# Optimization experiments

Measured on AMD Instinct MI355X. Metric: run time of the kernel, lower is better.

## Reference

```python
import jax, jax.numpy as jnp
import numpy as np
from jax import lax

B = 256
L = 1024
C = 64           # num_inputs == num_channels[l]
NUM_LAYERS = 5
KERNEL = 3
HID = 256
NUM_STATIC = 32
OUT_DIM = 2
KQ = 24576
T_TEMP = 0.07
NUM_NEIGHBORS = 1
EPS = 1e-12


def _l2n(x, axis):
    n = jnp.linalg.norm(x, axis=axis, keepdims=True)
    return x / jnp.maximum(n, EPS)


def _causal_conv(x, w, b, dil):
    # x: [B, C, L], w: [O, I, K] -> left-pad (K-1)*dil == Conv1d(pad both)+Chomp1d
    y = lax.conv_general_dilated(x, w, window_strides=(1,),
                                 padding=[((KERNEL - 1) * dil, 0)],
                                 rhs_dilation=(dil,),
                                 dimension_numbers=('NCH', 'OIH', 'NCH'))
    return y + b[None, :, None]


def _tcn(x, c1w, c1b, c2w, c2b):
    # stacked TemporalBlocks, dilation 2**l, identity residual (in==out channels)
    for l in range(NUM_LAYERS):
        d = 2 ** l
        h = jax.nn.relu(_causal_conv(x, c1w[l], c1b[l], d))
        h = jax.nn.relu(_causal_conv(h, c2w[l], c2b[l], d))
        x = jax.nn.relu(h + x)
    return x


def _mlp(x, w1, b1, w2, b2):
    # Linear -> ReLU -> Linear (use_batch_norm=False, eval: no dropout)
    return jax.nn.relu(x @ w1 + b1) @ w2 + b2


def setup_inputs() -> dict:
    key = jax.random.key(0)
    ks = jax.random.split(key, 24)
    d = {}
    d['sequence_q_s'] = jax.random.normal(ks[0], (B, L, C), jnp.float32)
    d['sequence_k_s'] = jax.random.normal(ks[1], (B, L, C), jnp.float32)
    d['static_s'] = jax.random.normal(ks[2], (B, NUM_STATIC), jnp.float32)
    d['sequence_q_t'] = jax.random.normal(ks[3], (B, L, C), jnp.float32)
    d['sequence_k_t'] = jax.random.normal(ks[4], (B, L, C), jnp.float32)
    d['static_t'] = jax.random.normal(ks[5], (B, NUM_STATIC), jnp.float32)
    d['alpha'] = jnp.ones((1,), jnp.float32)
    cs = 1.0 / np.sqrt(C * KERNEL)
    d['c1w'] = jax.random.normal(ks[6], (NUM_LAYERS, C, C, KERNEL), jnp.float32) * cs
    d['c1b'] = jnp.zeros((NUM_LAYERS, C), jnp.float32)
    d['c2w'] = jax.random.normal(ks[7], (NUM_LAYERS, C, C, KERNEL), jnp.float32) * cs
    d['c2b'] = jnp.zeros((NUM_LAYERS, C), jnp.float32)
    d['pjw1'] = jax.random.normal(ks[8], (C, HID), jnp.float32) / np.sqrt(C)
    d['pjb1'] = jnp.zeros((HID,), jnp.float32)
    d['pjw2'] = jax.random.normal(ks[9], (HID, C), jnp.float32) / np.sqrt(HID)
    d['pjb2'] = jnp.zeros((C,), jnp.float32)
    d['prw1'] = jax.random.normal(ks[10], (C + NUM_STATIC, HID), jnp.float32) / np.sqrt(C + NUM_STATIC)
    d['prb1'] = jnp.zeros((HID,), jnp.float32)
    d['prw2'] = jax.random.normal(ks[11], (HID, OUT_DIM), jnp.float32) / np.sqrt(HID)
    d['prb2'] = jnp.zeros((OUT_DIM,), jnp.float32)
    d['dw1'] = jax.random.normal(ks[12], (C, HID), jnp.float32) / np.sqrt(C)
    d['db1'] = jnp.zeros((HID,), jnp.float32)
    d['dw2'] = jax.random.normal(ks[13], (HID, 1), jnp.float32) / np.sqrt(HID)
    d['db2'] = jnp.zeros((1,), jnp.float32)
    qs = jax.random.normal(ks[14], (C, KQ), jnp.float32)
    qt = jax.random.normal(ks[15], (C, KQ), jnp.float32)
    d['queue_s'] = _l2n(qs, 0)
    d['queue_t'] = _l2n(qt, 0)
    return d


def reference(sequence_q_s, sequence_k_s, static_s, sequence_q_t, sequence_k_t, static_t, alpha,
              c1w, c1b, c2w, c2b, pjw1, pjb1, pjw2, pjb2, prw1, prb1, prw2, prb2,
              dw1, db1, dw2, db2, queue_s, queue_t):
    sg = lax.stop_gradient

    def encode(seq):  # [B, L, C] -> normalized [B, C]
        return _l2n(_tcn(jnp.transpose(seq, (0, 2, 1)), c1w, c1b, c2w, c2b)[:, :, -1], 1)

    q_s = encode(sequence_q_s)
    p_q_s = _l2n(_mlp(q_s, pjw1, pjb1, pjw2, pjb2), 1)
    q_t = encode(sequence_q_t)
    p_q_t = _l2n(_mlp(q_t, pjw1, pjb1, pjw2, pjb2), 1)
    # key encoder under no_grad (params equal to query encoder at init)
    k_s = sg(encode(sequence_k_s))
    k_t = sg(encode(sequence_k_t))

    logits_s = jnp.concatenate([p_q_s @ k_s.T, p_q_s @ sg(queue_s)], axis=1) / T_TEMP
    labels_s = jnp.arange(B, dtype=jnp.int32)
    logits_t = jnp.concatenate([p_q_t @ k_t.T, p_q_t @ sg(queue_t)], axis=1) / T_TEMP
    labels_t = jnp.arange(B, dtype=jnp.int32)

    # NN(k_t, q_s.detach()): cdist + topk smallest -> pseudo labels
    q_s_det = sg(q_s)
    d2 = (jnp.sum(k_t * k_t, 1)[:, None] + jnp.sum(q_s_det * q_s_det, 1)[None, :]
          - 2.0 * (k_t @ q_s_det.T))  # [B_t, B_s]
    _, idx = lax.top_k(-d2, NUM_NEIGHBORS)
    labels_ts = idx[:, 0]

    logits_ts = (q_t @ q_s_det.T) / T_TEMP

    labels_domain = jnp.concatenate([jnp.ones((B, 1), jnp.float32), jnp.zeros((B, 1), jnp.float32)], 0)
    # gradient reversal is identity in forward
    q_rev = jnp.concatenate([q_s, q_t], axis=0)
    pred_domain = _mlp(q_rev, dw1, db1, dw2, db2)

    y_s = _mlp(jnp.concatenate([q_s, static_s], axis=1), prw1, prb1, prw2, prb2)

    return (logits_s, labels_s, logits_t, labels_t, logits_ts, labels_ts,
            pred_domain, labels_domain, y_s)
```

## Files before the change

kernel.cpp:

```cpp
#include <hip/hip_runtime.h>
#include <hip/hip_bf16.h>

#define B_SZ   256
#define L_SZ   1024
#define C_SZ   64
#define HID    256
#define KQ     24576
#define WIN    125
#define WSTART (L_SZ - WIN)

#define OFF_LOGITS_S   0LL
#define OFF_LABELS_S   6356992LL
#define OFF_LOGITS_T   6357248LL
#define OFF_LABELS_T   12714240LL
#define OFF_LOGITS_TS  12714496LL
#define OFF_LABELS_TS  12780032LL
#define OFF_PRED_DOM   12780288LL
#define OFF_LABELS_DOM 12780800LL
#define OFF_YS         12781312LL

#define INV_T (1.0f / 0.07f)

typedef __attribute__((ext_vector_type(8))) short  bf16x8;
typedef __attribute__((ext_vector_type(4))) float  floatx4;
typedef __attribute__((ext_vector_type(16))) float floatx16;
typedef __attribute__((ext_vector_type(4))) unsigned short ushortx4;

__device__ __forceinline__ unsigned short f2bf_rne(float x) {
    unsigned u = __float_as_uint(x);
    unsigned r = u + 0x7fffu + ((u >> 16) & 1u);
    return (unsigned short)(r >> 16);
}
__device__ __forceinline__ float bf2f(unsigned short h) {
    return __uint_as_float(((unsigned)h) << 16);
}

__device__ __forceinline__ int swz2(int r) { return ((r >> 1) & 7) << 4; }

__global__ void prep_frag_kernel(const float* __restrict__ c1w,
                                 const float* __restrict__ c2w,
                                 unsigned short* __restrict__ wf) {
    int bid = blockIdx.x;
    int kb = bid & 1, mt = (bid >> 1) & 3;
    int sttap = bid >> 3;
    int tap = sttap % 3, st = sttap / 3;
    int l = st >> 1, cv = st & 1;
    int tid = threadIdx.x;
    int j = tid & 7, lane = tid >> 3;
    int co = mt * 16 + (lane & 15);
    int ci = kb * 32 + (lane >> 4) * 8 + j;
    const float* src = cv ? c2w : c1w;
    float w = src[((l * 64 + co) * 64 + ci) * 3 + tap];
    unsigned short hi = f2bf_rne(w);
    unsigned short lo = f2bf_rne(w - bf2f(hi));
    size_t b0 = ((((size_t)((st * 3 + tap) * 2 + 0)) * 4 + mt) * 2 + kb) * 512 + lane * 8 + j;
    size_t b1 = ((((size_t)((st * 3 + tap) * 2 + 1)) * 4 + mt) * 2 + kb) * 512 + lane * 8 + j;
    wf[b0] = hi;
    wf[b1] = lo;
}

#define R0H 0
#define R0L 16384
#define R1H 32768
#define R1L 40960
#define HHB 49152
#define HLB 65536
#define SCRATCH_B 57344

template<bool RES, bool FINAL>
__device__ __forceinline__ void conv_pass(
    char* lds, const bf16x8* __restrict__ wf8,
    int st, int inH, int inL, int rows_valid, int stride,
    int outH, int outL, int n_out, int tiles,
    int resH, int resL, int res_valid,
    const float* __restrict__ bias,
    int mt, int lg, int li, int lane)
{
    bf16x8 A[3][2][2];
#pragma unroll
    for (int tap = 0; tap < 3; ++tap)
#pragma unroll
        for (int h = 0; h < 2; ++h)
#pragma unroll
            for (int kb = 0; kb < 2; ++kb)
                A[tap][h][kb] = wf8[((((st * 3 + tap) * 2 + h) * 4 + mt) * 2 + kb) * 64 + lane];

    int co0 = mt * 16 + lg * 4;
    float4 b4 = *(const float4*)(bias + co0);
    float ba[4] = {b4.x, b4.y, b4.z, b4.w};

    for (int tt = 0; tt < tiles; ++tt) {
        int i = tt * 16 + li;
        floatx4 acc = {0.f, 0.f, 0.f, 0.f};
#pragma unroll
        for (int tap = 0; tap < 3; ++tap) {
            int jr = i * stride + tap;
            jr = (jr < rows_valid - 1) ? jr : (rows_valid - 1);
            int sw = swz2(jr);
            const char* pH = lds + inH + jr * 128;
            const char* pL = lds + inL + jr * 128;
#pragma unroll
            for (int kb = 0; kb < 2; ++kb) {
                int cb = (kb * 64 + lg * 16) ^ sw;
                bf16x8 bH = *(const bf16x8*)(pH + cb);
                bf16x8 bL = *(const bf16x8*)(pL + cb);
                acc = __builtin_amdgcn_mfma_f32_16x16x32_bf16(A[tap][0][kb], bH, acc, 0, 0, 0);
                acc = __builtin_amdgcn_mfma_f32_16x16x32_bf16(A[tap][0][kb], bL, acc, 0, 0, 0);
                acc = __builtin_amdgcn_mfma_f32_16x16x32_bf16(A[tap][1][kb], bH, acc, 0, 0, 0);
            }
        }
        float v[4];
#pragma unroll
        for (int r = 0; r < 4; ++r) v[r] = fmaxf(acc[r] + ba[r], 0.f);
        if (RES) {
            int rr = 2 * i + 4;
            rr = (rr < res_valid - 1) ? rr : (res_valid - 1);
            int rsw = swz2(rr);
            int rcb = (mt * 32 + lg * 8) ^ rsw;
            ushortx4 rh = *(const ushortx4*)(lds + resH + rr * 128 + rcb);
            ushortx4 rl = *(const ushortx4*)(lds + resL + rr * 128 + rcb);
#pragma unroll
            for (int r = 0; r < 4; ++r)
                v[r] = fmaxf(v[r] + bf2f(rh[r]) + bf2f(rl[r]), 0.f);
        }
        if (FINAL) {
            if (i == 0) {
                float* scratch = (float*)(lds + SCRATCH_B);
#pragma unroll
                for (int r = 0; r < 4; ++r) scratch[co0 + r] = v[r];
            }
        } else {
            if (i < n_out) {
                ushortx4 h4, l4;
#pragma unroll
                for (int r = 0; r < 4; ++r) {
                    unsigned short hh = f2bf_rne(v[r]);
                    h4[r] = (short)hh;
                    l4[r] = (short)f2bf_rne(v[r] - bf2f(hh));
                }
                int wsw = swz2(i);
                int wcb = (mt * 32 + lg * 8) ^ wsw;
                *(ushortx4*)(lds + outH + i * 128 + wcb) = h4;
                *(ushortx4*)(lds + outL + i * 128 + wcb) = l4;
            }
        }
    }
}

__launch_bounds__(256)
__global__ void encode_kernel(const float* __restrict__ sqs, const float* __restrict__ sks,
                              const float* __restrict__ sqt, const float* __restrict__ skt,
                              const unsigned short* __restrict__ wf,
                              const float* __restrict__ c1b, const float* __restrict__ c2b,
                              const float* __restrict__ pjw1, const float* __restrict__ pjb1,
                              const float* __restrict__ pjw2, const float* __restrict__ pjb2,
                              float* __restrict__ enc, float* __restrict__ proj,
                              unsigned short* __restrict__ pbf) {
    __shared__ char lds[81920];
    int b = blockIdx.x;
    int s = blockIdx.y;
    const float* seq = (s == 0) ? sqs : (s == 1) ? sks : (s == 2) ? sqt : skt;
    const float4* base4 = reinterpret_cast<const float4*>(seq + ((size_t)b * L_SZ + WSTART) * C_SZ);
    int tid = threadIdx.x;

    for (int idx = tid; idx < 2000; idx += 256) {
        float4 v = base4[idx];
        int t = idx >> 4, c0 = (idx & 15) * 4;
        int cb = (c0 * 2) ^ swz2(t);
        float vv[4] = {v.x, v.y, v.z, v.w};
        ushortx4 h4, l4;
#pragma unroll
        for (int r = 0; r < 4; ++r) {
            unsigned short hh = f2bf_rne(vv[r]);
            h4[r] = (short)hh;
            l4[r] = (short)f2bf_rne(vv[r] - bf2f(hh));
        }
        *(ushortx4*)(lds + R0H + t * 128 + cb) = h4;
        *(ushortx4*)(lds + R0L + t * 128 + cb) = l4;
    }
    __syncthreads();

    int mt   = tid >> 6;
    int lane = tid & 63;
    int lg = lane >> 4, li = lane & 15;
    const bf16x8* wf8 = (const bf16x8*)wf;

    const int n_in[5] = {125, 61, 29, 13, 5};
    const int n1a[5]  = {123, 59, 27, 11, 3};
    const int n2a[5]  = {61, 29, 13, 5, 1};
    const int t1a[5]  = {8, 4, 2, 1, 1};
    const int t2a[5]  = {4, 2, 1, 1, 1};

#pragma unroll
    for (int l = 0; l < 5; ++l) {
        int xH = (l & 1) ? R1H : R0H, xL = (l & 1) ? R1L : R0L;
        int yH = (l & 1) ? R0H : R1H, yL = (l & 1) ? R0L : R1L;
        conv_pass<false, false>(lds, wf8, l * 2, xH, xL, n_in[l], 1,
                                HHB, HLB, n1a[l], t1a[l], 0, 0, 0,
                                c1b + l * 64, mt, lg, li, lane);
        __syncthreads();
        if (l < 4) {
            conv_pass<true, false>(lds, wf8, l * 2 + 1, HHB, HLB, n1a[l], 2,
                                   yH, yL, n2a[l], t2a[l], xH, xL, n_in[l],
                                   c2b + l * 64, mt, lg, li, lane);
        } else {
            conv_pass<true, true>(lds, wf8, l * 2 + 1, HHB, HLB, n1a[l], 2,
                                  yH, yL, n2a[l], t2a[l], xH, xL, n_in[l],
                                  c2b + l * 64, mt, lg, li, lane);
        }
        __syncthreads();
    }

    float* xn = (float*)(lds + R0H);
    if (tid < 64) {
        float vv = ((float*)(lds + SCRATCH_B))[tid];
        float sq = vv * vv;
#pragma unroll
        for (int off = 32; off; off >>= 1) sq += __shfl_xor(sq, off, 64);
        float norm = fmaxf(sqrtf(sq), 1e-12f);
        float nv = vv / norm;
        enc[((size_t)s * B_SZ + b) * 64 + tid] = nv;
        xn[tid] = nv;
    }
    __syncthreads();

    if (s == 0 || s == 2) {
        float* hv   = (float*)(lds + R1H);
        float* red4 = (float*)(lds + R1H + 1024);
        {
            float acc = pjb1[tid];
            const float* wcol = pjw1 + tid;
            for (int c = 0; c < 64; ++c) acc = fmaf(xn[c], wcol[c * 256], acc);
            hv[tid] = fmaxf(acc, 0.f);
        }
        __syncthreads();
        {
            int wv = tid >> 6, o = tid & 63;
            float acc = 0.f;
            const float* wcol = pjw2 + o;
            int j0 = wv * 64;
            for (int j = j0; j < j0 + 64; ++j) acc = fmaf(hv[j], wcol[j * 64], acc);
            red4[wv * 64 + o] = acc;
        }
        __syncthreads();
        if (tid < 64) {
            float o = pjb2[tid];
#pragma unroll
            for (int k = 0; k < 4; ++k) o += red4[k * 64 + tid];
            float sq = o * o;
#pragma unroll
            for (int off = 32; off; off >>= 1) sq += __shfl_xor(sq, off, 64);
            float norm = fmaxf(sqrtf(sq), 1e-12f);
            float pv = o / norm;
            int which = s >> 1;
            proj[((size_t)which * B_SZ + b) * 64 + tid] = pv;
            pbf[((size_t)which * B_SZ + b) * 64 + tid] = f2bf_rne(pv);
        }
    }
}

__launch_bounds__(512)
__global__ void qlogits_kernel(const float* __restrict__ proj,
                               const unsigned short* __restrict__ pbf,
                               const float* __restrict__ enc,
                               const float* __restrict__ queue_s, const float* __restrict__ queue_t,
                               float* __restrict__ out) {
    __shared__ char lds[8448];
    int bx = blockIdx.x;
    int sz = blockIdx.y;
    int tid = threadIdx.x;
    long long outBase0 = (sz == 0) ? OFF_LOGITS_S : OFF_LOGITS_T;

    if (bx >= 384) {
        float (*pt)[65] = (float(*)[65])lds;
        int rt = bx - 384;
        const float* p = proj + ((size_t)sz * B_SZ + rt * 32) * 64;
        for (int idx = tid; idx < 32 * 64; idx += 512) {
            pt[idx >> 6][idx & 63] = p[idx];
        }
        __syncthreads();
        if (tid < 256) {
            float acc[32];
#pragma unroll
            for (int r = 0; r < 32; ++r) acc[r] = 0.f;
            int j = tid;
            const float* k = enc + ((size_t)(sz == 0 ? 1 : 3) * B_SZ + j) * 64;
            for (int c = 0; c < 64; ++c) {
                float bv = k[c];
#pragma unroll
                for (int r = 0; r < 32; ++r) acc[r] = fmaf(pt[r][c], bv, acc[r]);
            }
#pragma unroll
            for (int r = 0; r < 32; ++r) {
                out[outBase0 + (long long)(rt * 32 + r) * 24832 + j] = acc[r] * INV_T;
            }
        }
        return;
    }

    int j0 = bx * 64;
    const float* q = (sz == 0 ? queue_s : queue_t);

    {
#pragma unroll
        for (int pass = 0; pass < 2; ++pass) {
            int idx = pass * 512 + tid;
            int c = idx >> 4, jj0 = (idx & 15) * 4;
            float4 v = *(const float4*)(q + (size_t)c * KQ + j0 + jj0);
            float vv[4] = {v.x, v.y, v.z, v.w};
#pragma unroll
            for (int r = 0; r < 4; ++r) {
                int jj = jj0 + r;
                *(unsigned short*)(lds + jj * 128 + ((c * 2) ^ ((jj & 7) << 4))) = f2bf_rne(vv[r]);
            }
        }
    }
    __syncthreads();

    int w = tid >> 6, lane = tid & 63;
    int r31 = lane & 31, hi = lane >> 5;
    int arow = w * 32 + r31;
    const bf16x8* pa = (const bf16x8*)(pbf + ((size_t)sz * B_SZ + arow) * 64);
    bf16x8 A[4];
#pragma unroll
    for (int ks = 0; ks < 4; ++ks)
        A[ks] = pa[ks * 2 + hi];
    long long outBase = outBase0 + 256 + j0;
#pragma unroll
    for (int ct = 0; ct < 2; ++ct) {
        int col = ct * 32 + r31;
        bf16x8 Bf[4];
#pragma unroll
        for (int ks = 0; ks < 4; ++ks)
            Bf[ks] = *(const bf16x8*)(lds + col * 128 + (((ks * 16 + hi * 8) * 2) ^ ((col & 7) << 4)));
        floatx16 acc;
#pragma unroll
        for (int r = 0; r < 16; ++r) acc[r] = 0.f;
#pragma unroll
        for (int ks = 0; ks < 4; ++ks)
            acc = __builtin_amdgcn_mfma_f32_32x32x16_bf16(A[ks], Bf[ks], acc, 0, 0, 0);
#pragma unroll
        for (int r = 0; r < 16; ++r) {
            int drow = (r & 3) + 8 * (r >> 2) + 4 * hi;
            out[outBase + (long long)(w * 32 + drow) * 24832 + ct * 32 + r31] = acc[r] * INV_T;
        }
    }
}

__global__ void heads_kernel(const float* __restrict__ enc, const float* __restrict__ stat,
                             const float* __restrict__ dw1, const float* __restrict__ db1,
                             const float* __restrict__ dw2, const float* __restrict__ db2,
                             const float* __restrict__ prw1, const float* __restrict__ prb1,
                             const float* __restrict__ prw2, const float* __restrict__ prb2,
                             float* __restrict__ out) {
    int bx = blockIdx.x;
    int tid = threadIdx.x;

    if (bx < 256) {
        __shared__ float kt[64];
        __shared__ float qt[64];
        __shared__ float swv[4];
        __shared__ int   swj[4];
        int i = bx;
        if (tid < 64) {
            kt[tid] = enc[((size_t)3 * B_SZ + i) * 64 + tid];
            qt[tid] = enc[((size_t)2 * B_SZ + i) * 64 + tid];
        }
        __syncthreads();
        int j = tid;
        const float* qs = enc + (size_t)j * 64;
        float dkt = 0.f, dqt = 0.f, qq = 0.f, kk = 0.f;
        for (int c = 0; c < 64; ++c) {
            float v = qs[c];
            dkt = fmaf(kt[c], v, dkt);
            dqt = fmaf(qt[c], v, dqt);
            qq  = fmaf(v, v, qq);
            kk  = fmaf(kt[c], kt[c], kk);
        }
        out[OFF_LOGITS_TS + (long long)i * 256 + j] = dqt * INV_T;
        float d2 = kk + qq - 2.f * dkt;
        float bv = d2; int bj = j;
#pragma unroll
        for (int off = 32; off; off >>= 1) {
            float ov = __shfl_xor(bv, off, 64);
            int   oj = __shfl_xor(bj, off, 64);
            if (ov < bv || (ov == bv && oj < bj)) { bv = ov; bj = oj; }
        }
        int w = tid >> 6;
        if ((tid & 63) == 0) { swv[w] = bv; swj[w] = bj; }
        __syncthreads();
        if (tid == 0) {
            float best = swv[0]; int bi = swj[0];
#pragma unroll
            for (int k = 1; k < 4; ++k)
                if (swv[k] < best || (swv[k] == best && swj[k] < bi)) { best = swv[k]; bi = swj[k]; }
            out[OFF_LABELS_TS + i] = (float)bi;
        }
    } else if (bx < 768) {
        __shared__ float xv[64];
        __shared__ float red[256];
        int r = bx - 256;
        const float* x = enc + ((r < 256) ? ((size_t)0 * B_SZ + r) : ((size_t)2 * B_SZ + (r - 256))) * 64;
        if (tid < 64) xv[tid] = x[tid];
        __syncthreads();
        float h = db1[tid];
        for (int c = 0; c < 64; ++c) h = fmaf(xv[c], dw1[c * 256 + tid], h);
        h = fmaxf(h, 0.f);
        red[tid] = h * dw2[tid];
        __syncthreads();
        for (int s = 128; s; s >>= 1) {
            if (tid < s) red[tid] += red[tid + s];
            __syncthreads();
        }
        if (tid == 0) out[OFF_PRED_DOM + r] = red[0] + db2[0];
    } else if (bx < 1024) {
        __shared__ float xv[96];
        __shared__ float red[256];
        int b = bx - 768;
        if (tid < 64)       xv[tid] = enc[(size_t)b * 64 + tid];
        else if (tid < 96)  xv[tid] = stat[(size_t)b * 32 + (tid - 64)];
        __syncthreads();
        float h = prb1[tid];
        for (int c = 0; c < 96; ++c) h = fmaf(xv[c], prw1[c * 256 + tid], h);
        h = fmaxf(h, 0.f);
        for (int o = 0; o < 2; ++o) {
            red[tid] = h * prw2[tid * 2 + o];
            __syncthreads();
            for (int s = 128; s; s >>= 1) {
                if (tid < s) red[tid] += red[tid + s];
                __syncthreads();
            }
            if (tid == 0) out[OFF_YS + (long long)b * 2 + o] = red[0] + prb2[o];
            __syncthreads();
        }
    } else {
        int t = (bx - 1024) * 256 + tid;
        if (t < 256) {
            out[OFF_LABELS_S + t] = (float)t;
            out[OFF_LABELS_T + t] = (float)t;
        }
        if (t < 512) out[OFF_LABELS_DOM + t] = (t < 256) ? 1.f : 0.f;
    }
}

extern "C" void kernel_launch(void* const* d_in, const int* in_sizes, int n_in,
                              void* d_out, int out_size, void* d_ws, size_t ws_size,
                              hipStream_t stream) {
    const float* sqs    = (const float*)d_in[0];
    const float* sks    = (const float*)d_in[1];
    const float* stat_s = (const float*)d_in[2];
    const float* sqt    = (const float*)d_in[3];
    const float* skt    = (const float*)d_in[4];
    const float* c1w    = (const float*)d_in[7];
    const float* c1b    = (const float*)d_in[8];
    const float* c2w    = (const float*)d_in[9];
    const float* c2b    = (const float*)d_in[10];
    const float* pjw1   = (const float*)d_in[11];
    const float* pjb1   = (const float*)d_in[12];
    const float* pjw2   = (const float*)d_in[13];
    const float* pjb2   = (const float*)d_in[14];
    const float* prw1   = (const float*)d_in[15];
    const float* prb1   = (const float*)d_in[16];
    const float* prw2   = (const float*)d_in[17];
    const float* prb2   = (const float*)d_in[18];
    const float* dw1    = (const float*)d_in[19];
    const float* db1    = (const float*)d_in[20];
    const float* dw2    = (const float*)d_in[21];
    const float* db2    = (const float*)d_in[22];
    const float* queue_s = (const float*)d_in[23];
    const float* queue_t = (const float*)d_in[24];

    float* out = (float*)d_out;
    unsigned short* wf = (unsigned short*)d_ws;
    float* enc  = (float*)((char*)d_ws + 491520);
    float* proj = enc + 65536;
    unsigned short* pbf = (unsigned short*)(proj + 32768);

    prep_frag_kernel<<<240, 512, 0, stream>>>(c1w, c2w, wf);
    encode_kernel<<<dim3(256, 4), 256, 0, stream>>>(sqs, sks, sqt, skt, wf, c1b, c2b,
                                                    pjw1, pjb1, pjw2, pjb2, enc, proj, pbf);
    qlogits_kernel<<<dim3(392, 2), 512, 0, stream>>>(proj, pbf, enc, queue_s, queue_t, out);
    heads_kernel<<<1026, 256, 0, stream>>>(enc, stat_s, dw1, db1, dw2, db2,
                                           prw1, prb1, prw2, prb2, out);
}
```

Baseline: 89.23 us.

## Split TCN encoder into two kernels, batching four sequences per block for late layers

The encoder kernel is split in two. The first kernel runs layers 0-1 per sequence and spills the layer-2 input (29 rows, split into hi and lo bf16 halves) into the output buffer as scratch. The second kernel packs four sequences per block for layers 2-4 and the projection MLP, so the tiny late layers with only one or two tiles no longer leave most waves idle. The price is an extra launch and a global round trip, and the LDS swizzle is changed from pairs of rows to single rows.

```diff
diff --git a/kernel.cpp b/kernel.cpp
--- a/kernel.cpp
+++ b/kernel.cpp
@@ -35,7 +35,7 @@
     return __uint_as_float(((unsigned)h) << 16);
 }
 
-__device__ __forceinline__ int swz2(int r) { return ((r >> 1) & 7) << 4; }
+__device__ __forceinline__ int swzl(int r) { return (r & 7) << 4; }
 
 __global__ void prep_frag_kernel(const float* __restrict__ c1w,
                                  const float* __restrict__ c2w,
@@ -65,97 +65,104 @@
 #define R1L 40960
 #define HHB 49152
 #define HLB 65536
-#define SCRATCH_B 57344
 
 template<bool RES, bool FINAL>
-__device__ __forceinline__ void conv_pass(
-    char* lds, const bf16x8* __restrict__ wf8,
-    int st, int inH, int inL, int rows_valid, int stride,
+__device__ __forceinline__ void conv_tile(
+    char* L, const bf16x8 A[3][2][2],
+    int inH, int inL, int rows_valid, int stride,
+    int outH, int outL, int n_out, int scrOff,
+    int resH, int resL, int res_valid,
+    const float ba[4], int i, int mt, int lg)
+{
+    floatx4 acc = {0.f, 0.f, 0.f, 0.f};
+#pragma unroll
+    for (int tap = 0; tap < 3; ++tap) {
+        int jr = i * stride + tap;
+        jr = (jr < rows_valid - 1) ? jr : (rows_valid - 1);
+        int sw = swzl(jr);
+        const char* pH = L + inH + jr * 128;
+        const char* pL = L + inL + jr * 128;
+#pragma unroll
+        for (int kb = 0; kb < 2; ++kb) {
+            int cb = (kb * 64 + lg * 16) ^ sw;
+            bf16x8 bH = *(const bf16x8*)(pH + cb);
+            bf16x8 bL = *(const bf16x8*)(pL + cb);
+            acc = __builtin_amdgcn_mfma_f32_16x16x32_bf16(A[tap][0][kb], bH, acc, 0, 0, 0);
+            acc = __builtin_amdgcn_mfma_f32_16x16x32_bf16(A[tap][0][kb], bL, acc, 0, 0, 0);
+            acc = __builtin_amdgcn_mfma_f32_16x16x32_bf16(A[tap][1][kb], bH, acc, 0, 0, 0);
+        }
+    }
+    float v[4];
+#pragma unroll
+    for (int r = 0; r < 4; ++r) v[r] = fmaxf(acc[r] + ba[r], 0.f);
+    if (RES) {
+        int rr = 2 * i + 4;
+        rr = (rr < res_valid - 1) ? rr : (res_valid - 1);
+        int rcb = (mt * 32 + lg * 8) ^ swzl(rr);
+        ushortx4 rh = *(const ushortx4*)(L + resH + rr * 128 + rcb);
+        ushortx4 rl = *(const ushortx4*)(L + resL + rr * 128 + rcb);
+#pragma unroll
+        for (int r = 0; r < 4; ++r)
+            v[r] = fmaxf(v[r] + bf2f(rh[r]) + bf2f(rl[r]), 0.f);
+    }
+    if (FINAL) {
+        if (i == 0) {
+            float* scr = (float*)(L + scrOff);
+            int co0 = mt * 16 + lg * 4;
+#pragma unroll
+            for (int r = 0; r < 4; ++r) scr[co0 + r] = v[r];
+        }
+    } else if (i < n_out) {
+        ushortx4 h4, l4;
+#pragma unroll
+        for (int r = 0; r < 4; ++r) {
+            unsigned short hh = f2bf_rne(v[r]);
+            h4[r] = (short)hh;
+            l4[r] = (short)f2bf_rne(v[r] - bf2f(hh));
+        }
+        int wcb = (mt * 32 + lg * 8) ^ swzl(i);
+        *(ushortx4*)(L + outH + i * 128 + wcb) = h4;
+        *(ushortx4*)(L + outL + i * 128 + wcb) = l4;
+    }
+}
+
+__device__ __forceinline__ void loadAfrag(bf16x8 A[3][2][2], const bf16x8* __restrict__ wf8,
+                                          int st, int mt, int lane) {
+#pragma unroll
+    for (int tap = 0; tap < 3; ++tap)
+#pragma unroll
+        for (int h = 0; h < 2; ++h)
+#pragma unroll
+            for (int kb = 0; kb < 2; ++kb)
+                A[tap][h][kb] = wf8[((((st * 3 + tap) * 2 + h) * 4 + mt) * 2 + kb) * 64 + lane];
+}
+
+template<bool RES>
+__device__ __forceinline__ void conv_passA(
+    char* lds, const bf16x8* __restrict__ wf8, int st,
+    int inH, int inL, int rows_valid, int stride,
     int outH, int outL, int n_out, int tiles,
     int resH, int resL, int res_valid,
-    const float* __restrict__ bias,
-    int mt, int lg, int li, int lane)
+    const float* __restrict__ bias, int mt, int lg, int li, int lane)
 {
     bf16x8 A[3][2][2];
-#pragma unroll
-    for (int tap = 0; tap < 3; ++tap)
-#pragma unroll
-        for (int h = 0; h < 2; ++h)
-#pragma unroll
-            for (int kb = 0; kb < 2; ++kb)
-                A[tap][h][kb] = wf8[((((st * 3 + tap) * 2 + h) * 4 + mt) * 2 + kb) * 64 + lane];
-
+    loadAfrag(A, wf8, st, mt, lane);
     int co0 = mt * 16 + lg * 4;
     float4 b4 = *(const float4*)(bias + co0);
     float ba[4] = {b4.x, b4.y, b4.z, b4.w};
-
     for (int tt = 0; tt < tiles; ++tt) {
-        int i = tt * 16 + li;
-        floatx4 acc = {0.f, 0.f, 0.f, 0.f};
-#pragma unroll
-        for (int tap = 0; tap < 3; ++tap) {
-            int jr = i * stride + tap;
-            jr = (jr < rows_valid - 1) ? jr : (rows_valid - 1);
-            int sw = swz2(jr);
-            const char* pH = lds + inH + jr * 128;
-            const char* pL = lds + inL + jr * 128;
-#pragma unroll
-            for (int kb = 0; kb < 2; ++kb) {
-                int cb = (kb * 64 + lg * 16) ^ sw;
-                bf16x8 bH = *(const bf16x8*)(pH + cb);
-                bf16x8 bL = *(const bf16x8*)(pL + cb);
-                acc = __builtin_amdgcn_mfma_f32_16x16x32_bf16(A[tap][0][kb], bH, acc, 0, 0, 0);
-                acc = __builtin_amdgcn_mfma_f32_16x16x32_bf16(A[tap][0][kb], bL, acc, 0, 0, 0);
-                acc = __builtin_amdgcn_mfma_f32_16x16x32_bf16(A[tap][1][kb], bH, acc, 0, 0, 0);
-            }
-        }
-        float v[4];
-#pragma unroll
-        for (int r = 0; r < 4; ++r) v[r] = fmaxf(acc[r] + ba[r], 0.f);
-        if (RES) {
-            int rr = 2 * i + 4;
-            rr = (rr < res_valid - 1) ? rr : (res_valid - 1);
-            int rsw = swz2(rr);
-            int rcb = (mt * 32 + lg * 8) ^ rsw;
-            ushortx4 rh = *(const ushortx4*)(lds + resH + rr * 128 + rcb);
-            ushortx4 rl = *(const ushortx4*)(lds + resL + rr * 128 + rcb);
-#pragma unroll
-            for (int r = 0; r < 4; ++r)
-                v[r] = fmaxf(v[r] + bf2f(rh[r]) + bf2f(rl[r]), 0.f);
-        }
-        if (FINAL) {
-            if (i == 0) {
-                float* scratch = (float*)(lds + SCRATCH_B);
-#pragma unroll
-                for (int r = 0; r < 4; ++r) scratch[co0 + r] = v[r];
-            }
-        } else {
-            if (i < n_out) {
-                ushortx4 h4, l4;
-#pragma unroll
-                for (int r = 0; r < 4; ++r) {
-                    unsigned short hh = f2bf_rne(v[r]);
-                    h4[r] = (short)hh;
-                    l4[r] = (short)f2bf_rne(v[r] - bf2f(hh));
-                }
-                int wsw = swz2(i);
-                int wcb = (mt * 32 + lg * 8) ^ wsw;
-                *(ushortx4*)(lds + outH + i * 128 + wcb) = h4;
-                *(ushortx4*)(lds + outL + i * 128 + wcb) = l4;
-            }
-        }
+        conv_tile<RES, false>(lds, A, inH, inL, rows_valid, stride,
+                              outH, outL, n_out, 0, resH, resL, res_valid,
+                              ba, tt * 16 + li, mt, lg);
     }
 }
 
 __launch_bounds__(256)
-__global__ void encode_kernel(const float* __restrict__ sqs, const float* __restrict__ sks,
-                              const float* __restrict__ sqt, const float* __restrict__ skt,
-                              const unsigned short* __restrict__ wf,
-                              const float* __restrict__ c1b, const float* __restrict__ c2b,
-                              const float* __restrict__ pjw1, const float* __restrict__ pjb1,
-                              const float* __restrict__ pjw2, const float* __restrict__ pjb2,
-                              float* __restrict__ enc, float* __restrict__ proj,
-                              unsigned short* __restrict__ pbf) {
+__global__ void encodeA_kernel(const float* __restrict__ sqs, const float* __restrict__ sks,
+                               const float* __restrict__ sqt, const float* __restrict__ skt,
+                               const unsigned short* __restrict__ wf,
+                               const float* __restrict__ c1b, const float* __restrict__ c2b,
+                               char* __restrict__ x2) {
     __shared__ char lds[81920];
     int b = blockIdx.x;
     int s = blockIdx.y;
@@ -166,7 +173,7 @@
     for (int idx = tid; idx < 2000; idx += 256) {
         float4 v = base4[idx];
         int t = idx >> 4, c0 = (idx & 15) * 4;
-        int cb = (c0 * 2) ^ swz2(t);
+        int cb = (c0 * 2) ^ swzl(t);
         float vv[4] = {v.x, v.y, v.z, v.w};
         ushortx4 h4, l4;
 #pragma unroll
@@ -185,76 +192,159 @@
     int lg = lane >> 4, li = lane & 15;
     const bf16x8* wf8 = (const bf16x8*)wf;
 
-    const int n_in[5] = {125, 61, 29, 13, 5};
-    const int n1a[5]  = {123, 59, 27, 11, 3};
-    const int n2a[5]  = {61, 29, 13, 5, 1};
-    const int t1a[5]  = {8, 4, 2, 1, 1};
-    const int t2a[5]  = {4, 2, 1, 1, 1};
-
-#pragma unroll
-    for (int l = 0; l < 5; ++l) {
-        int xH = (l & 1) ? R1H : R0H, xL = (l & 1) ? R1L : R0L;
-        int yH = (l & 1) ? R0H : R1H, yL = (l & 1) ? R0L : R1L;
-        conv_pass<false, false>(lds, wf8, l * 2, xH, xL, n_in[l], 1,
-                                HHB, HLB, n1a[l], t1a[l], 0, 0, 0,
-                                c1b + l * 64, mt, lg, li, lane);
-        __syncthreads();
-        if (l < 4) {
-            conv_pass<true, false>(lds, wf8, l * 2 + 1, HHB, HLB, n1a[l], 2,
-                                   yH, yL, n2a[l], t2a[l], xH, xL, n_in[l],
-                                   c2b + l * 64, mt, lg, li, lane);
-        } else {
-            conv_pass<true, true>(lds, wf8, l * 2 + 1, HHB, HLB, n1a[l], 2,
-                                  yH, yL, n2a[l], t2a[l], xH, xL, n_in[l],
-                                  c2b + l * 64, mt, lg, li, lane);
-        }
-        __syncthreads();
-    }
-
-    float* xn = (float*)(lds + R0H);
-    if (tid < 64) {
-        float vv = ((float*)(lds + SCRATCH_B))[tid];
+    conv_passA<false>(lds, wf8, 0, R0H, R0L, 125, 1, HHB, HLB, 123, 8, 0, 0, 0,
+                      c1b, mt, lg, li, lane);
+    __syncthreads();
+    conv_passA<true>(lds, wf8, 1, HHB, HLB, 123, 2, R1H, R1L, 61, 4, R0H, R0L, 125,
+                     c2b, mt, lg, li, lane);
+    __syncthreads();
+    conv_passA<false>(lds, wf8, 2, R1H, R1L, 61, 1, HHB, HLB, 59, 4, 0, 0, 0,
+                      c1b + 64, mt, lg, li, lane);
+    __syncthreads();
+    conv_passA<true>(lds, wf8, 3, HHB, HLB, 59, 2, R0H, R0L, 29, 2, R1H, R1L, 61,
+                     c2b + 64, mt, lg, li, lane);
+    __syncthreads();
+
+    char* dst = x2 + (size_t)(s * 256 + b) * 7424;
+    for (int idx = tid; idx < 928; idx += 256) {
+        int p = idx / 464, rr = idx % 464;
+        int r = rr >> 4, ch = rr & 15;
+        const char* src = lds + (p ? R0L : R0H) + r * 128 + ((ch * 8) ^ swzl(r));
+        *(ushortx4*)(dst + p * 3712 + r * 128 + ch * 8) = *(const ushortx4*)src;
+    }
+}
+
+#define ITEM_B 17920
+#define BR0H 0
+#define BR0L 3712
+#define BR1H 7424
+#define BR1L 9088
+#define BHH  10752
+#define BHL  14208
+#define BSCR 17664
+
+template<bool RES, bool FINAL>
+__device__ __forceinline__ void conv_passB(
+    char* lds, const bf16x8* __restrict__ wf8, int st,
+    int inH, int inL, int rows_valid, int stride,
+    int outH, int outL, int n_out, int tiles,
+    int resH, int resL, int res_valid,
+    const float* __restrict__ bias, int mt, int lg, int li, int lane)
+{
+    bf16x8 A[3][2][2];
+    loadAfrag(A, wf8, st, mt, lane);
+    int co0 = mt * 16 + lg * 4;
+    float4 b4 = *(const float4*)(bias + co0);
+    float ba[4] = {b4.x, b4.y, b4.z, b4.w};
+#pragma unroll
+    for (int it = 0; it < 4; ++it) {
+        char* L = lds + it * ITEM_B;
+        for (int tt = 0; tt < tiles; ++tt) {
+            conv_tile<RES, FINAL>(L, A, inH, inL, rows_valid, stride,
+                                  outH, outL, n_out, BSCR, resH, resL, res_valid,
+                                  ba, tt * 16 + li, mt, lg);
+        }
+    }
+}
+
+__launch_bounds__(256)
+__global__ void encodeB_kernel(const char* __restrict__ x2,
+                               const unsigned short* __restrict__ wf,
+                               const float* __restrict__ c1b, const float* __restrict__ c2b,
+                               const float* __restrict__ pjw1, const float* __restrict__ pjb1,
+                               const float* __restrict__ pjw2, const float* __restrict__ pjb2,
+                               float* __restrict__ enc, float* __restrict__ proj,
+                               unsigned short* __restrict__ pbf) {
+    __shared__ char lds[71680];
+    int bx = blockIdx.x;
+    int s  = blockIdx.y;
+    int tid = threadIdx.x;
+
+    for (int idx = tid; idx < 3712; idx += 256) {
+        int it = idx / 928, rem = idx % 928;
+        int p = rem / 464, rr = rem % 464;
+        int r = rr >> 4, ch = rr & 15;
+        const char* src = x2 + (size_t)(s * 256 + bx * 4 + it) * 7424 + p * 3712 + r * 128 + ch * 8;
+        char* dst = lds + it * ITEM_B + (p ? BR0L : BR0H) + r * 128 + ((ch * 8) ^ swzl(r));
+        *(ushortx4*)dst = *(const ushortx4*)src;
+    }
+    __syncthreads();
+
+    int mt   = tid >> 6;
+    int lane = tid & 63;
+    int lg = lane >> 4, li = lane & 15;
+    const bf16x8* wf8 = (const bf16x8*)wf;
+
+    conv_passB<false, false>(lds, wf8, 4, BR0H, BR0L, 29, 1, BHH, BHL, 27, 2, 0, 0, 0,
+                             c1b + 128, mt, lg, li, lane);
+    __syncthreads();
+    conv_passB<true, false>(lds, wf8, 5, BHH, BHL, 27, 2, BR1H, BR1L, 13, 1, BR0H, BR0L, 29,
+                            c2b + 128, mt, lg, li, lane);
+    __syncthreads();
+    conv_passB<false, false>(lds, wf8, 6, BR1H, BR1L, 13, 1, BHH, BHL, 11, 1, 0, 0, 0,
+                             c1b + 192, mt, lg, li, lane);
+    __syncthreads();
+    conv_passB<true, false>(lds, wf8, 7, BHH, BHL, 11, 2, BR0H, BR0L, 5, 1, BR1H, BR1L, 13,
+                            c2b + 192, mt, lg, li, lane);
+    __syncthreads();
+    conv_passB<false, false>(lds, wf8, 8, BR0H, BR0L, 5, 1, BHH, BHL, 3, 1, 0, 0, 0,
+                             c1b + 256, mt, lg, li, lane);
+    __syncthreads();
+    conv_passB<true, true>(lds, wf8, 9, BHH, BHL, 3, 2, BR1H, BR1L, 1, 1, BR0H, BR0L, 5,
+                           c2b + 256, mt, lg, li, lane);
+    __syncthreads();
+
+    {
+        float* scr = (float*)(lds + mt * ITEM_B + BSCR);
+        float vv = scr[lane];
         float sq = vv * vv;
 #pragma unroll
         for (int off = 32; off; off >>= 1) sq += __shfl_xor(sq, off, 64);
         float norm = fmaxf(sqrtf(sq), 1e-12f);
         float nv = vv / norm;
-        enc[((size_t)s * B_SZ + b) * 64 + tid] = nv;
-        xn[tid] = nv;
+        int item = bx * 4 + mt;
+        enc[((size_t)s * B_SZ + item) * 64 + lane] = nv;
+        scr[lane] = nv;
     }
     __syncthreads();
 
     if (s == 0 || s == 2) {
-        float* hv   = (float*)(lds + R1H);
-        float* red4 = (float*)(lds + R1H + 1024);
-        {
-            float acc = pjb1[tid];
-            const float* wcol = pjw1 + tid;
-            for (int c = 0; c < 64; ++c) acc = fmaf(xn[c], wcol[c * 256], acc);
-            hv[tid] = fmaxf(acc, 0.f);
-        }
-        __syncthreads();
-        {
-            int wv = tid >> 6, o = tid & 63;
-            float acc = 0.f;
-            const float* wcol = pjw2 + o;
-            int j0 = wv * 64;
-            for (int j = j0; j < j0 + 64; ++j) acc = fmaf(hv[j], wcol[j * 64], acc);
-            red4[wv * 64 + o] = acc;
-        }
-        __syncthreads();
-        if (tid < 64) {
-            float o = pjb2[tid];
-#pragma unroll
-            for (int k = 0; k < 4; ++k) o += red4[k * 64 + tid];
-            float sq = o * o;
-#pragma unroll
-            for (int off = 32; off; off >>= 1) sq += __shfl_xor(sq, off, 64);
-            float norm = fmaxf(sqrtf(sq), 1e-12f);
-            float pv = o / norm;
-            int which = s >> 1;
-            proj[((size_t)which * B_SZ + b) * 64 + tid] = pv;
-            pbf[((size_t)which * B_SZ + b) * 64 + tid] = f2bf_rne(pv);
+        int which = s >> 1;
+        for (int it = 0; it < 4; ++it) {
+            char* L = lds + it * ITEM_B;
+            const float* xn = (const float*)(L + BSCR);
+            float* hv   = (float*)(L + BR1H);
+            float* red4 = (float*)(L + BR1L);
+            {
+                float acc = pjb1[tid];
+                const float* wcol = pjw1 + tid;
+                for (int c = 0; c < 64; ++c) acc = fmaf(xn[c], wcol[c * 256], acc);
+                hv[tid] = fmaxf(acc, 0.f);
+            }
+            __syncthreads();
+            {
+                int wv = tid >> 6, o = tid & 63;
+                float acc = 0.f;
+                const float* wcol = pjw2 + o;
+                int j0 = wv * 64;
+                for (int j = j0; j < j0 + 64; ++j) acc = fmaf(hv[j], wcol[j * 64], acc);
+                red4[wv * 64 + o] = acc;
+            }
+            __syncthreads();
+            if (tid < 64) {
+                float o = pjb2[tid];
+#pragma unroll
+                for (int k = 0; k < 4; ++k) o += red4[k * 64 + tid];
+                float sq = o * o;
+#pragma unroll
+                for (int off = 32; off; off >>= 1) sq += __shfl_xor(sq, off, 64);
+                float norm = fmaxf(sqrtf(sq), 1e-12f);
+                float pv = o / norm;
+                int item = bx * 4 + it;
+                proj[((size_t)which * B_SZ + item) * 64 + tid] = pv;
+                pbf[((size_t)which * B_SZ + item) * 64 + tid] = f2bf_rne(pv);
+            }
+            __syncthreads();
         }
     }
 }
@@ -300,7 +390,6 @@
 
     int j0 = bx * 64;
     const float* q = (sz == 0 ? queue_s : queue_t);
-
     {
 #pragma unroll
         for (int pass = 0; pass < 2; ++pass) {
@@ -475,9 +564,11 @@
     float* enc  = (float*)((char*)d_ws + 491520);
     float* proj = enc + 65536;
     unsigned short* pbf = (unsigned short*)(proj + 32768);
+    char* x2 = (char*)d_out;
 
     prep_frag_kernel<<<240, 512, 0, stream>>>(c1w, c2w, wf);
-    encode_kernel<<<dim3(256, 4), 256, 0, stream>>>(sqs, sks, sqt, skt, wf, c1b, c2b,
+    encodeA_kernel<<<dim3(256, 4), 256, 0, stream>>>(sqs, sks, sqt, skt, wf, c1b, c2b, x2);
+    encodeB_kernel<<<dim3(64, 4), 256, 0, stream>>>(x2, wf, c1b, c2b,
                                                     pjw1, pjb1, pjw2, pjb2, enc, proj, pbf);
     qlogits_kernel<<<dim3(392, 2), 512, 0, stream>>>(proj, pbf, enc, queue_s, queue_t, out);
     heads_kernel<<<1026, 256, 0, stream>>>(enc, stat_s, dw1, db1, dw2, db2,
```

Result: slower. 99.03 us (+11.0%).
